# Kernel optimization log

Hardware: AMD Instinct MI355X
Metric: run time of the kernel (lower is better)

## Reference

```python
import jax, jax.numpy as jnp
import numpy as np

B, D, N, K, V = 32, 256, 2048, 512, 6
COMMIT = 1.0

def setup_inputs() -> dict:
    key = jax.random.key(0)
    k1, k2 = jax.random.split(key)
    inputs = jax.random.normal(k1, (B, D, N), dtype=jnp.float32)
    embeddings = jax.random.normal(k2, (V, D, K), dtype=jnp.float32)
    return {"inputs": inputs, "embeddings": embeddings}

def _vq_layer(residual, emb):
    # residual: (B, D, N); emb: (D, K) codebook
    flat = residual.transpose(0, 2, 1).reshape(-1, D)                # (B*N, D)
    dist = (jnp.sum(flat * flat, axis=1, keepdims=True)
            + jnp.sum(emb * emb, axis=0, keepdims=True)
            - 2.0 * (flat @ emb))                                    # (B*N, K)
    idx = jnp.argmin(dist, axis=1)                                   # (B*N,)
    q = jnp.take(emb.T, idx, axis=0)                                 # (B*N, D) gather
    q = q.reshape(B, N, D).transpose(0, 2, 1)                        # (B, D, N)
    # straight-through estimator
    q_st = residual + jax.lax.stop_gradient(q - residual)
    loss = COMMIT * jnp.mean(jnp.square(jax.lax.stop_gradient(q) - residual))
    return q_st, idx.reshape(B, N), loss

def reference(inputs, embeddings):
    residual = inputs
    q_sum = jnp.zeros_like(inputs)
    tokens = []
    total_loss = jnp.float32(0.0)
    for v in range(V):  # fixed small layer stack
        q, idx, loss = _vq_layer(residual, embeddings[v])
        q_sum = q_sum + q
        tokens.append(idx)
        total_loss = total_loss + loss
        residual = residual - q
    return q_sum, jnp.stack(tokens, axis=0), total_loss
```

## Files before the change

kernel.cpp:

```cpp
#include <hip/hip_runtime.h>

#define B_  32
#define D_  256
#define N_  2048
#define K_  512
#define V_  6
#define DN_ (D_*N_)
#define DK_ (D_*K_)
#define QSZ (B_*D_*N_)
#define TOKSZ (B_*N_)
#define TOK_OFF QSZ
#define LOSS_OFF (QSZ + V_*TOKSZ)
#define MARGIN 0.02f
#define TPB 64
#define NBLK (TOKSZ/TPB)

typedef __attribute__((ext_vector_type(8))) short short8b;
typedef __attribute__((ext_vector_type(4))) float f32x4;

__device__ __forceinline__ unsigned short f2bf(float x) {
  unsigned u = __float_as_uint(x);
  unsigned r = (u + 0x7fffu + ((u >> 16) & 1u)) >> 16;
  return (unsigned short)r;
}
__device__ __forceinline__ float bf2f(unsigned short h) {
  return __uint_as_float(((unsigned)h) << 16);
}
__device__ __forceinline__ unsigned orderf(float f) {
  unsigned u = __float_as_uint(f);
  return (u >> 31) ? ~u : (u | 0x80000000u);
}
__device__ __forceinline__ float unorderf(unsigned u) {
  return __uint_as_float((u & 0x80000000u) ? (u & 0x7fffffffu) : ~u);
}
__device__ __forceinline__ unsigned long long shfl_xor_u64(unsigned long long v, int m) {
  int lo = __shfl_xor((int)(unsigned)(v & 0xffffffffull), m, 64);
  int hi = __shfl_xor((int)(unsigned)(v >> 32), m, 64);
  return ((unsigned long long)(unsigned)hi << 32) | (unsigned)lo;
}

__global__ __launch_bounds__(256) void pack_kernel(const float* __restrict__ emb,
                                                   float* __restrict__ Ef32,
                                                   unsigned short* __restrict__ Ehi,
                                                   unsigned short* __restrict__ Elo) {
  __shared__ float T[64][68];
  const int tid = threadIdx.x;
  const int k0 = blockIdx.x * 64, d0 = blockIdx.y * 64, v = blockIdx.z;
  const float* src = emb + (size_t)v * DK_;
  const int r = tid >> 4, c4 = (tid & 15) * 4;
  #pragma unroll
  for (int i = 0; i < 4; ++i) {
    int d = d0 + r + i * 16;
    float4 x = *(const float4*)(src + (size_t)d * K_ + k0 + c4);
    *(float4*)&T[r + i * 16][c4] = x;
  }
  __syncthreads();
  #pragma unroll
  for (int i = 0; i < 4; ++i) {
    int k = k0 + r + i * 16;
    float4 wv;
    wv.x = T[c4 + 0][r + i * 16];
    wv.y = T[c4 + 1][r + i * 16];
    wv.z = T[c4 + 2][r + i * 16];
    wv.w = T[c4 + 3][r + i * 16];
    size_t o = ((size_t)v * K_ + k) * 256 + d0 + c4;
    *(float4*)(Ef32 + o) = wv;
    ushort4 hv, lv;
    hv.x = f2bf(wv.x); lv.x = f2bf(wv.x - bf2f(hv.x));
    hv.y = f2bf(wv.y); lv.y = f2bf(wv.y - bf2f(hv.y));
    hv.z = f2bf(wv.z); lv.z = f2bf(wv.z - bf2f(hv.z));
    hv.w = f2bf(wv.w); lv.w = f2bf(wv.w - bf2f(hv.w));
    *(ushort4*)(Ehi + o) = hv;
    *(ushort4*)(Elo + o) = lv;
  }
}

__global__ __launch_bounds__(256) void en2_kernel(const float* __restrict__ Ef32,
                                                  float* __restrict__ en2f,
                                                  double* __restrict__ en2d) {
  __shared__ double P[64][4];
  const int tid = threadIdx.x;
  const int k = blockIdx.x * 64 + (tid >> 2), q = tid & 3;
  const float* e = Ef32 + (size_t)k * 256 + q * 64;
  double s = 0.0;
  #pragma unroll 8
  for (int i = 0; i < 64; ++i) { double x = (double)e[i]; s = fma(x, x, s); }
  P[tid >> 2][q] = s;
  __syncthreads();
  if (tid < 64) {
    int k2 = blockIdx.x * 64 + tid;
    double t = (P[tid][0] + P[tid][1]) + (P[tid][2] + P[tid][3]);
    en2d[k2] = t;
    en2f[k2] = (float)t;
  }
}

__global__ __launch_bounds__(256, 2) void rvq_fused(
    const float* __restrict__ inputs,
    const unsigned short* __restrict__ Ehi, const unsigned short* __restrict__ Elo,
    const float* __restrict__ Ef32, const float* __restrict__ en2f,
    const double* __restrict__ en2d,
    float* __restrict__ tokens, float* __restrict__ lossPart)
{
  __shared__ unsigned short Ahi[8 * 2048];
  __shared__ unsigned short Alo[8 * 2048];
  __shared__ unsigned long long wmin[4][TPB];
  __shared__ float wsec[4][TPB];
  __shared__ int sIdx[TPB];
  __shared__ int sHist[V_][TPB];
  __shared__ double rD[256];
  __shared__ double sbd[256];
  __shared__ int sbk[256];
  __shared__ unsigned long long sFlag;
  __shared__ float wred[4];

  const int tid = threadIdx.x;
  const int lane = tid & 63, w = tid >> 6;
  const int l15 = lane & 15, lg = lane >> 4;
  const int gt0 = blockIdx.x * TPB;
  const int b = gt0 >> 11, n0 = gt0 & (N_ - 1);
  const int kb = w * 128;

  {
    const float* src = inputs + (size_t)b * DN_ + n0 + lane;
    #pragma unroll
    for (int cc = 0; cc < 2; ++cc) {
      const int c = w * 2 + cc;
      #pragma unroll
      for (int g = 0; g < 4; ++g) {
        short8b hv, lv;
        #pragma unroll
        for (int e = 0; e < 8; ++e) {
          float x = src[(size_t)(c * 32 + g * 8 + e) * N_];
          unsigned short h = f2bf(x);
          hv[e] = (short)h;
          lv[e] = (short)f2bf(x - bf2f(h));
        }
        *(short8b*)&Ahi[c * 2048 + g * 512 + lane * 8] = hv;
        *(short8b*)&Alo[c * 2048 + g * 512 + lane * 8] = lv;
      }
    }
  }
  __syncthreads();

  for (int v = 0; v < V_; ++v) {
    const unsigned short* ehiL = Ehi + (size_t)v * DK_ + (size_t)(kb + l15) * 256 + lg * 8;
    const unsigned short* eloL = Elo + (size_t)v * DK_ + (size_t)(kb + l15) * 256 + lg * 8;
    const float* Ef32v = Ef32 + (size_t)v * DK_;

    f32x4 acc[4][8];
    #pragma unroll
    for (int tt = 0; tt < 4; ++tt)
      #pragma unroll
      for (int kt = 0; kt < 8; ++kt) acc[tt][kt] = (f32x4){0.f, 0.f, 0.f, 0.f};

    #pragma unroll
    for (int c = 0; c < 8; ++c) {
      short8b ah[4], al[4];
      #pragma unroll
      for (int tt = 0; tt < 4; ++tt) {
        ah[tt] = *(const short8b*)&Ahi[c * 2048 + lg * 512 + (tt * 16 + l15) * 8];
        al[tt] = *(const short8b*)&Alo[c * 2048 + lg * 512 + (tt * 16 + l15) * 8];
      }
      #pragma unroll
      for (int kt = 0; kt < 8; ++kt) {
        short8b bh = *(const short8b*)(ehiL + (size_t)kt * 4096 + c * 32);
        short8b bl = *(const short8b*)(eloL + (size_t)kt * 4096 + c * 32);
        #pragma unroll
        for (int tt = 0; tt < 4; ++tt) {
          acc[tt][kt] = __builtin_amdgcn_mfma_f32_16x16x32_bf16(ah[tt], bh, acc[tt][kt], 0, 0, 0);
          acc[tt][kt] = __builtin_amdgcn_mfma_f32_16x16x32_bf16(ah[tt], bl, acc[tt][kt], 0, 0, 0);
          acc[tt][kt] = __builtin_amdgcn_mfma_f32_16x16x32_bf16(al[tt], bh, acc[tt][kt], 0, 0, 0);
        }
      }
    }

    float en8[8];
    #pragma unroll
    for (int kt = 0; kt < 8; ++kt) en8[kt] = en2f[v * K_ + kb + kt * 16 + l15];

    #pragma unroll
    for (int tt = 0; tt < 4; ++tt)
      #pragma unroll
      for (int r = 0; r < 4; ++r) {
        const int token = tt * 16 + lg * 4 + r;
        float dv0 = en8[0] - 2.f * acc[tt][0][r];
        unsigned long long p = ((unsigned long long)orderf(dv0) << 32) | (unsigned)(kb + l15);
        float s = 3.402823466e+38f;
        #pragma unroll
        for (int kt = 1; kt < 8; ++kt) {
          float dv = en8[kt] - 2.f * acc[tt][kt][r];
          unsigned long long pk = ((unsigned long long)orderf(dv) << 32) |
                                  (unsigned)(kb + kt * 16 + l15);
          if (pk < p) { s = fminf(s, unorderf((unsigned)(p >> 32))); p = pk; }
          else s = fminf(s, dv);
        }
        #pragma unroll
        for (int m = 1; m <= 8; m <<= 1) {
          unsigned long long po = shfl_xor_u64(p, m);
          float so = __shfl_xor(s, m, 64);
          unsigned long long pmax = (po < p) ? p : po;
          s = fminf(fminf(s, so), unorderf((unsigned)(pmax >> 32)));
          p = (po < p) ? po : p;
        }
        if (l15 == 0) { wmin[w][token] = p; wsec[w][token] = s; }
      }
    __syncthreads();
    if (tid < TPB) {
      unsigned long long p = wmin[0][tid]; float s = wsec[0][tid];
      #pragma unroll
      for (int w2 = 1; w2 < 4; ++w2) {
        unsigned long long po = wmin[w2][tid]; float so = wsec[w2][tid];
        unsigned long long pmax = (po < p) ? p : po;
        s = fminf(fminf(s, so), unorderf((unsigned)(pmax >> 32)));
        p = (po < p) ? po : p;
      }
      sIdx[tid] = (int)(p & 0xffffffffull);
      float bd = unorderf((unsigned)(p >> 32));
      unsigned long long fl = __ballot(s - bd < MARGIN);
      if (tid == 0) sFlag = fl;
    }
    __syncthreads();

    unsigned long long mask = sFlag;
    while (mask) {
      const int j = __builtin_ctzll(mask);
      mask &= mask - 1;
      double r = (double)inputs[(size_t)b * DN_ + (size_t)tid * N_ + (n0 + j)];
      for (int u = 0; u < v; ++u)
        r -= (double)Ef32[(size_t)u * DK_ + (size_t)sHist[u][j] * 256 + tid];
      rD[tid] = r;
      __syncthreads();
      double best = 1.0e300; int bk = 0;
      #pragma unroll
      for (int half = 0; half < 2; ++half) {
        const int k = tid + half * 256;
        const float* e0 = Ef32v + (size_t)k * 256;
        double s0 = 0.0, s1 = 0.0, s2 = 0.0, s3 = 0.0;
        #pragma unroll 8
        for (int dd = 0; dd < 256; dd += 4) {
          s0 = fma(rD[dd + 0], (double)e0[dd + 0], s0);
          s1 = fma(rD[dd + 1], (double)e0[dd + 1], s1);
          s2 = fma(rD[dd + 2], (double)e0[dd + 2], s2);
          s3 = fma(rD[dd + 3], (double)e0[dd + 3], s3);
        }
        double dist = en2d[v * K_ + k] - 2.0 * ((s0 + s1) + (s2 + s3));
        if (dist < best) { best = dist; bk = k; }
      }
      sbd[tid] = best; sbk[tid] = bk;
      __syncthreads();
      for (int st = 128; st >= 1; st >>= 1) {
        if (tid < st) {
          double od = sbd[tid + st]; int ok = sbk[tid + st];
          if (od < sbd[tid] || (od == sbd[tid] && ok < sbk[tid])) {
            sbd[tid] = od; sbk[tid] = ok;
          }
        }
        __syncthreads();
      }
      if (tid == 0) sIdx[j] = sbk[0];
      __syncthreads();
    }

    if (tid < TPB) {
      sHist[v][tid] = sIdx[tid];
      tokens[(size_t)v * TOKSZ + gt0 + tid] = (float)sIdx[tid];
    }
    __syncthreads();

    const int uj = tid >> 2, q = tid & 3;
    const int kw = sIdx[uj];
    const float* er = Ef32v + (size_t)kw * 256 + q * 64;
    float lacc = 0.f;
    #pragma unroll
    for (int i = 0; i < 8; ++i) {
      const int c = q * 2 + (i >> 2), g = i & 3;
      unsigned short* ph = &Ahi[c * 2048 + g * 512 + uj * 8];
      unsigned short* pl = &Alo[c * 2048 + g * 512 + uj * 8];
      short8b h8 = *(const short8b*)ph;
      short8b l8 = *(const short8b*)pl;
      float4 e0 = *(const float4*)(er + i * 8);
      float4 e1 = *(const float4*)(er + i * 8 + 4);
      float ee[8] = {e0.x, e0.y, e0.z, e0.w, e1.x, e1.y, e1.z, e1.w};
      short8b nh, nl;
      #pragma unroll
      for (int jj = 0; jj < 8; ++jj) {
        float rv = bf2f((unsigned short)h8[jj]) + bf2f((unsigned short)l8[jj]);
        float rn = rv - ee[jj];
        unsigned short hh = f2bf(rn);
        nh[jj] = (short)hh;
        nl[jj] = (short)f2bf(rn - bf2f(hh));
        lacc += rn * rn;
      }
      if (v < V_ - 1) {
        *(short8b*)ph = nh;
        *(short8b*)pl = nl;
      }
    }
    #pragma unroll
    for (int m = 32; m >= 1; m >>= 1) lacc += __shfl_xor(lacc, m, 64);
    if (lane == 0) wred[w] = lacc;
    __syncthreads();
    if (tid == 0)
      lossPart[(size_t)v * NBLK + blockIdx.x] = (wred[0] + wred[1]) + (wred[2] + wred[3]);
    __syncthreads();
  }
}

__global__ __launch_bounds__(256) void finalize_q(const float* __restrict__ toks,
                                                  const float* __restrict__ Ef32,
                                                  float* __restrict__ out) {
  const int tid = threadIdx.x;
  const int gt = blockIdx.x * 64 + (tid >> 2);
  const int q = tid & 3;
  const int b = gt >> 11, n = gt & (N_ - 1);
  float4 a[16];
  int k0 = (int)toks[gt];
  const float* e0 = Ef32 + (size_t)k0 * 256 + q * 64;
  #pragma unroll
  for (int i = 0; i < 16; ++i) a[i] = ((const float4*)e0)[i];
  #pragma unroll
  for (int v = 1; v < V_; ++v) {
    int kv = (int)toks[v * TOKSZ + gt];
    const float* ev = Ef32 + (size_t)v * DK_ + (size_t)kv * 256 + q * 64;
    #pragma unroll
    for (int i = 0; i < 16; ++i) {
      float4 e = ((const float4*)ev)[i];
      a[i].x += e.x; a[i].y += e.y; a[i].z += e.z; a[i].w += e.w;
    }
  }
  float* dst = out + (size_t)b * DN_ + n;
  #pragma unroll
  for (int i = 0; i < 16; ++i) {
    int d = q * 64 + i * 4;
    dst[(size_t)(d + 0) * N_] = a[i].x;
    dst[(size_t)(d + 1) * N_] = a[i].y;
    dst[(size_t)(d + 2) * N_] = a[i].z;
    dst[(size_t)(d + 3) * N_] = a[i].w;
  }
}

__global__ __launch_bounds__(256) void loss_kernel(const float* __restrict__ part,
                                                   float* __restrict__ out) {
  __shared__ float s[256];
  const int tid = threadIdx.x;
  float a = 0.f;
  for (int i = tid; i < V_ * NBLK; i += 256) a += part[i];
  s[tid] = a;
  __syncthreads();
  for (int st = 128; st >= 1; st >>= 1) {
    if (tid < st) s[tid] += s[tid + st];
    __syncthreads();
  }
  if (tid == 0) out[LOSS_OFF] = s[0] * (1.0f / (float)QSZ);
}

extern "C" void kernel_launch(void* const* d_in, const int* in_sizes, int n_in,
                              void* d_out, int out_size, void* d_ws, size_t ws_size,
                              hipStream_t stream) {
  (void)in_sizes; (void)n_in; (void)out_size; (void)ws_size;
  const float* inputs = (const float*)d_in[0];
  const float* emb    = (const float*)d_in[1];
  float* out = (float*)d_out;
  char* ws = (char*)d_ws;

  unsigned short* Ehi = (unsigned short*)(ws + 0);
  unsigned short* Elo = (unsigned short*)(ws + 1572864);
  float*  Ef32 = (float*)(ws + 3145728);
  float*  en2f = (float*)(ws + 6291456);
  double* en2d = (double*)(ws + 6303744);
  float*  part = (float*)(ws + 6328320);

  float* toks = out + TOK_OFF;

  pack_kernel<<<dim3(8, 4, 6), 256, 0, stream>>>(emb, Ef32, Ehi, Elo);
  en2_kernel<<<48, 256, 0, stream>>>(Ef32, en2f, en2d);
  rvq_fused<<<NBLK, 256, 0, stream>>>(inputs, Ehi, Elo, Ef32, en2f, en2d, toks, part);
  finalize_q<<<TOKSZ / 64, 256, 0, stream>>>(toks, Ef32, out);
  loss_kernel<<<1, 256, 0, stream>>>(part, out);
}
```

Before: 730.4 us.

## Defer near-tie fp64 rechecks to a separate fixup kernel and halve token tile

Result: slower. 1.201 ms (+64.4%).

```diff
diff --git a/kernel.cpp b/kernel.cpp
--- a/kernel.cpp
+++ b/kernel.cpp
@@ -12,7 +12,8 @@
 #define TOK_OFF QSZ
 #define LOSS_OFF (QSZ + V_*TOKSZ)
 #define MARGIN 0.02f
-#define TPB 64
+#define FCAP 32768
+#define TPB 32
 #define NBLK (TOKSZ/TPB)
 
 typedef __attribute__((ext_vector_type(8))) short short8b;
@@ -95,23 +96,18 @@
   }
 }
 
-__global__ __launch_bounds__(256, 2) void rvq_fused(
+__global__ __launch_bounds__(256, 4) void rvq_fused(
     const float* __restrict__ inputs,
     const unsigned short* __restrict__ Ehi, const unsigned short* __restrict__ Elo,
     const float* __restrict__ Ef32, const float* __restrict__ en2f,
-    const double* __restrict__ en2d,
-    float* __restrict__ tokens, float* __restrict__ lossPart)
+    float* __restrict__ tokens, float* __restrict__ lossPart,
+    int* __restrict__ flagCnt, int* __restrict__ flagList)
 {
-  __shared__ unsigned short Ahi[8 * 2048];
-  __shared__ unsigned short Alo[8 * 2048];
+  __shared__ unsigned short Ahi[8 * 1024];
+  __shared__ unsigned short Alo[8 * 1024];
   __shared__ unsigned long long wmin[4][TPB];
   __shared__ float wsec[4][TPB];
   __shared__ int sIdx[TPB];
-  __shared__ int sHist[V_][TPB];
-  __shared__ double rD[256];
-  __shared__ double sbd[256];
-  __shared__ int sbk[256];
-  __shared__ unsigned long long sFlag;
   __shared__ float wred[4];
 
   const int tid = threadIdx.x;
@@ -122,23 +118,20 @@
   const int kb = w * 128;
 
   {
-    const float* src = inputs + (size_t)b * DN_ + n0 + lane;
-    #pragma unroll
-    for (int cc = 0; cc < 2; ++cc) {
-      const int c = w * 2 + cc;
-      #pragma unroll
-      for (int g = 0; g < 4; ++g) {
-        short8b hv, lv;
-        #pragma unroll
-        for (int e = 0; e < 8; ++e) {
-          float x = src[(size_t)(c * 32 + g * 8 + e) * N_];
-          unsigned short h = f2bf(x);
-          hv[e] = (short)h;
-          lv[e] = (short)f2bf(x - bf2f(h));
-        }
-        *(short8b*)&Ahi[c * 2048 + g * 512 + lane * 8] = hv;
-        *(short8b*)&Alo[c * 2048 + g * 512 + lane * 8] = lv;
-      }
+    const int tok = tid & 31, c = tid >> 5;
+    const float* src = inputs + (size_t)b * DN_ + n0 + tok;
+    #pragma unroll
+    for (int g = 0; g < 4; ++g) {
+      short8b hv, lv;
+      #pragma unroll
+      for (int e = 0; e < 8; ++e) {
+        float x = src[(size_t)(c * 32 + g * 8 + e) * N_];
+        unsigned short h = f2bf(x);
+        hv[e] = (short)h;
+        lv[e] = (short)f2bf(x - bf2f(h));
+      }
+      *(short8b*)&Ahi[c * 1024 + g * 256 + tok * 8] = hv;
+      *(short8b*)&Alo[c * 1024 + g * 256 + tok * 8] = lv;
     }
   }
   __syncthreads();
@@ -148,30 +141,28 @@
     const unsigned short* eloL = Elo + (size_t)v * DK_ + (size_t)(kb + l15) * 256 + lg * 8;
     const float* Ef32v = Ef32 + (size_t)v * DK_;
 
-    f32x4 acc[4][8];
-    #pragma unroll
-    for (int tt = 0; tt < 4; ++tt)
+    f32x4 acc[2][8];
+    #pragma unroll
+    for (int tt = 0; tt < 2; ++tt)
       #pragma unroll
       for (int kt = 0; kt < 8; ++kt) acc[tt][kt] = (f32x4){0.f, 0.f, 0.f, 0.f};
 
     #pragma unroll
     for (int c = 0; c < 8; ++c) {
-      short8b ah[4], al[4];
-      #pragma unroll
-      for (int tt = 0; tt < 4; ++tt) {
-        ah[tt] = *(const short8b*)&Ahi[c * 2048 + lg * 512 + (tt * 16 + l15) * 8];
-        al[tt] = *(const short8b*)&Alo[c * 2048 + lg * 512 + (tt * 16 + l15) * 8];
-      }
+      short8b ah0 = *(const short8b*)&Ahi[c * 1024 + lg * 256 + l15 * 8];
+      short8b ah1 = *(const short8b*)&Ahi[c * 1024 + lg * 256 + (16 + l15) * 8];
+      short8b al0 = *(const short8b*)&Alo[c * 1024 + lg * 256 + l15 * 8];
+      short8b al1 = *(const short8b*)&Alo[c * 1024 + lg * 256 + (16 + l15) * 8];
       #pragma unroll
       for (int kt = 0; kt < 8; ++kt) {
         short8b bh = *(const short8b*)(ehiL + (size_t)kt * 4096 + c * 32);
         short8b bl = *(const short8b*)(eloL + (size_t)kt * 4096 + c * 32);
-        #pragma unroll
-        for (int tt = 0; tt < 4; ++tt) {
-          acc[tt][kt] = __builtin_amdgcn_mfma_f32_16x16x32_bf16(ah[tt], bh, acc[tt][kt], 0, 0, 0);
-          acc[tt][kt] = __builtin_amdgcn_mfma_f32_16x16x32_bf16(ah[tt], bl, acc[tt][kt], 0, 0, 0);
-          acc[tt][kt] = __builtin_amdgcn_mfma_f32_16x16x32_bf16(al[tt], bh, acc[tt][kt], 0, 0, 0);
-        }
+        acc[0][kt] = __builtin_amdgcn_mfma_f32_16x16x32_bf16(ah0, bh, acc[0][kt], 0, 0, 0);
+        acc[0][kt] = __builtin_amdgcn_mfma_f32_16x16x32_bf16(ah0, bl, acc[0][kt], 0, 0, 0);
+        acc[0][kt] = __builtin_amdgcn_mfma_f32_16x16x32_bf16(al0, bh, acc[0][kt], 0, 0, 0);
+        acc[1][kt] = __builtin_amdgcn_mfma_f32_16x16x32_bf16(ah1, bh, acc[1][kt], 0, 0, 0);
+        acc[1][kt] = __builtin_amdgcn_mfma_f32_16x16x32_bf16(ah1, bl, acc[1][kt], 0, 0, 0);
+        acc[1][kt] = __builtin_amdgcn_mfma_f32_16x16x32_bf16(al1, bh, acc[1][kt], 0, 0, 0);
       }
     }
 
@@ -180,7 +171,7 @@
     for (int kt = 0; kt < 8; ++kt) en8[kt] = en2f[v * K_ + kb + kt * 16 + l15];
 
     #pragma unroll
-    for (int tt = 0; tt < 4; ++tt)
+    for (int tt = 0; tt < 2; ++tt)
       #pragma unroll
       for (int r = 0; r < 4; ++r) {
         const int token = tt * 16 + lg * 4 + r;
@@ -215,27 +206,77 @@
         s = fminf(fminf(s, so), unorderf((unsigned)(pmax >> 32)));
         p = (po < p) ? po : p;
       }
-      sIdx[tid] = (int)(p & 0xffffffffull);
+      int kwin = (int)(p & 0xffffffffull);
+      sIdx[tid] = kwin;
+      tokens[(size_t)v * TOKSZ + gt0 + tid] = (float)kwin;
       float bd = unorderf((unsigned)(p >> 32));
-      unsigned long long fl = __ballot(s - bd < MARGIN);
-      if (tid == 0) sFlag = fl;
-    }
-    __syncthreads();
-
-    unsigned long long mask = sFlag;
-    while (mask) {
-      const int j = __builtin_ctzll(mask);
-      mask &= mask - 1;
-      double r = (double)inputs[(size_t)b * DN_ + (size_t)tid * N_ + (n0 + j)];
-      for (int u = 0; u < v; ++u)
-        r -= (double)Ef32[(size_t)u * DK_ + (size_t)sHist[u][j] * 256 + tid];
-      rD[tid] = r;
-      __syncthreads();
+      if (s - bd < MARGIN) {
+        int pos = atomicAdd(flagCnt, 1);
+        if (pos < FCAP) flagList[pos] = gt0 + tid;
+      }
+    }
+    __syncthreads();
+
+    const int uj = tid >> 3, q = tid & 7;
+    const int kw = sIdx[uj];
+    const float* er = Ef32v + (size_t)kw * 256 + q * 32;
+    float lacc = 0.f;
+    #pragma unroll
+    for (int g = 0; g < 4; ++g) {
+      unsigned short* ph = &Ahi[q * 1024 + g * 256 + uj * 8];
+      unsigned short* pl = &Alo[q * 1024 + g * 256 + uj * 8];
+      short8b h8 = *(const short8b*)ph;
+      short8b l8 = *(const short8b*)pl;
+      float4 e0 = *(const float4*)(er + g * 8);
+      float4 e1 = *(const float4*)(er + g * 8 + 4);
+      float ee[8] = {e0.x, e0.y, e0.z, e0.w, e1.x, e1.y, e1.z, e1.w};
+      short8b nh, nl;
+      #pragma unroll
+      for (int jj = 0; jj < 8; ++jj) {
+        float rv = bf2f((unsigned short)h8[jj]) + bf2f((unsigned short)l8[jj]);
+        float rn = rv - ee[jj];
+        unsigned short hh = f2bf(rn);
+        nh[jj] = (short)hh;
+        nl[jj] = (short)f2bf(rn - bf2f(hh));
+        lacc += rn * rn;
+      }
+      if (v < V_ - 1) {
+        *(short8b*)ph = nh;
+        *(short8b*)pl = nl;
+      }
+    }
+    #pragma unroll
+    for (int m = 32; m >= 1; m >>= 1) lacc += __shfl_xor(lacc, m, 64);
+    if (lane == 0) wred[w] = lacc;
+    __syncthreads();
+    if (tid == 0)
+      lossPart[(size_t)v * NBLK + blockIdx.x] = (wred[0] + wred[1]) + (wred[2] + wred[3]);
+    __syncthreads();
+  }
+}
+
+__global__ __launch_bounds__(256) void chain_fixup(
+    const float* __restrict__ inputs, const float* __restrict__ Ef32,
+    const double* __restrict__ en2d, float* __restrict__ tokens,
+    const int* __restrict__ flagList, const int* __restrict__ flagCnt)
+{
+  __shared__ double rD[256];
+  __shared__ double sbd[256];
+  __shared__ int sbk[256];
+  const int tid = threadIdx.x;
+  int cnt = flagCnt[0]; if (cnt > FCAP) cnt = FCAP;
+  for (int i = blockIdx.x; i < cnt; i += gridDim.x) {
+    const int gt = flagList[i];
+    const int b = gt >> 11, n = gt & (N_ - 1);
+    rD[tid] = (double)inputs[(size_t)b * DN_ + (size_t)tid * N_ + n];
+    __syncthreads();
+    for (int v = 0; v < V_; ++v) {
+      const float* Ev = Ef32 + (size_t)v * DK_;
       double best = 1.0e300; int bk = 0;
       #pragma unroll
       for (int half = 0; half < 2; ++half) {
         const int k = tid + half * 256;
-        const float* e0 = Ef32v + (size_t)k * 256;
+        const float* e0 = Ev + (size_t)k * 256;
         double s0 = 0.0, s1 = 0.0, s2 = 0.0, s3 = 0.0;
         #pragma unroll 8
         for (int dd = 0; dd < 256; dd += 4) {
@@ -258,52 +299,13 @@
         }
         __syncthreads();
       }
-      if (tid == 0) sIdx[j] = sbk[0];
+      const int nk = sbk[0];
+      if (tid == 0) tokens[(size_t)v * TOKSZ + gt] = (float)nk;
+      double e = (double)Ev[(size_t)nk * 256 + tid];
       __syncthreads();
-    }
-
-    if (tid < TPB) {
-      sHist[v][tid] = sIdx[tid];
-      tokens[(size_t)v * TOKSZ + gt0 + tid] = (float)sIdx[tid];
-    }
-    __syncthreads();
-
-    const int uj = tid >> 2, q = tid & 3;
-    const int kw = sIdx[uj];
-    const float* er = Ef32v + (size_t)kw * 256 + q * 64;
-    float lacc = 0.f;
-    #pragma unroll
-    for (int i = 0; i < 8; ++i) {
-      const int c = q * 2 + (i >> 2), g = i & 3;
-      unsigned short* ph = &Ahi[c * 2048 + g * 512 + uj * 8];
-      unsigned short* pl = &Alo[c * 2048 + g * 512 + uj * 8];
-      short8b h8 = *(const short8b*)ph;
-      short8b l8 = *(const short8b*)pl;
-      float4 e0 = *(const float4*)(er + i * 8);
-      float4 e1 = *(const float4*)(er + i * 8 + 4);
-      float ee[8] = {e0.x, e0.y, e0.z, e0.w, e1.x, e1.y, e1.z, e1.w};
-      short8b nh, nl;
-      #pragma unroll
-      for (int jj = 0; jj < 8; ++jj) {
-        float rv = bf2f((unsigned short)h8[jj]) + bf2f((unsigned short)l8[jj]);
-        float rn = rv - ee[jj];
-        unsigned short hh = f2bf(rn);
-        nh[jj] = (short)hh;
-        nl[jj] = (short)f2bf(rn - bf2f(hh));
-        lacc += rn * rn;
-      }
-      if (v < V_ - 1) {
-        *(short8b*)ph = nh;
-        *(short8b*)pl = nl;
-      }
-    }
-    #pragma unroll
-    for (int m = 32; m >= 1; m >>= 1) lacc += __shfl_xor(lacc, m, 64);
-    if (lane == 0) wred[w] = lacc;
-    __syncthreads();
-    if (tid == 0)
-      lossPart[(size_t)v * NBLK + blockIdx.x] = (wred[0] + wred[1]) + (wred[2] + wred[3]);
-    __syncthreads();
+      rD[tid] = rD[tid] - e;
+      __syncthreads();
+    }
   }
 }
 
@@ -370,12 +372,17 @@
   float*  en2f = (float*)(ws + 6291456);
   double* en2d = (double*)(ws + 6303744);
   float*  part = (float*)(ws + 6328320);
+  int*    flagCnt  = (int*)(ws + 6377472);
+  int*    flagList = (int*)(ws + 6377476);
 
   float* toks = out + TOK_OFF;
 
+  hipMemsetAsync(flagCnt, 0, sizeof(int), stream);
   pack_kernel<<<dim3(8, 4, 6), 256, 0, stream>>>(emb, Ef32, Ehi, Elo);
   en2_kernel<<<48, 256, 0, stream>>>(Ef32, en2f, en2d);
-  rvq_fused<<<NBLK, 256, 0, stream>>>(inputs, Ehi, Elo, Ef32, en2f, en2d, toks, part);
+  rvq_fused<<<NBLK, 256, 0, stream>>>(inputs, Ehi, Elo, Ef32, en2f,
+                                      toks, part, flagCnt, flagList);
+  chain_fixup<<<2048, 256, 0, stream>>>(inputs, Ef32, en2d, toks, flagList, flagCnt);
   finalize_q<<<TOKSZ / 64, 256, 0, stream>>>(toks, Ef32, out);
   loss_kernel<<<1, 256, 0, stream>>>(part, out);
 }
```
